# Optimization experiments

Measured on AMD Instinct MI355X. Metric: run time of the kernel, lower is better.

## Reference

```python
import jax, jax.numpy as jnp
import numpy as np

N = 1_000_000
DEG = 10          # max_output_degree
IN = 16           # in_size (must equal rank for the original einsum to be valid)
RANK = 16
OUT = 16


def setup_inputs() -> dict:
    key = jax.random.key(0)
    k_ns, k_u0, k_ur, k_uo = jax.random.split(key, 4)
    neighbour_states = jax.random.normal(k_ns, (N, DEG, IN), dtype=jnp.float32)
    # Original init uses th.rand (uniform [0,1)).
    U0 = jax.random.uniform(k_u0, (IN, RANK), dtype=jnp.float32)
    U_rest = jax.random.uniform(k_ur, (DEG - 1, IN, RANK, RANK), dtype=jnp.float32)
    U_output = jax.random.uniform(k_uo, (RANK, OUT), dtype=jnp.float32)
    return {"neighbour_states": neighbour_states, "U0": U0, "U_rest": U_rest, "U_output": U_output}


def reference(neighbour_states, U0, U_rest, U_output):
    # neighbour_states: [N, DEG, IN]
    h0 = neighbour_states[:, 0, :]                      # [N, IN]
    ris0 = jnp.einsum('bc,nb->nc', U0, h0)              # [N, RANK]
    hs = jnp.moveaxis(neighbour_states[:, 1:, :], 1, 0)  # [DEG-1, N, IN]

    def step(ris, inputs):
        U, h = inputs                                   # U: [IN, RANK, RANK] (IN==RANK), h: [N, IN]
        ris = jnp.einsum('abc,na,nb->nc', U, ris, h)    # [N, RANK]
        return ris, None

    ris, _ = jax.lax.scan(step, ris0, (U_rest, hs))
    h_out = jnp.einsum('ab,na->nb', U_output, ris)      # [N, OUT]
    return h_out
```

## Files before the change

### kernel.cpp

```cpp
#include <hip/hip_runtime.h>

#define NSTEP 9

typedef __attribute__((ext_vector_type(8)))  __bf16 bf16x8;
typedef __attribute__((ext_vector_type(8)))  short  short8;
typedef __attribute__((ext_vector_type(4)))  float  floatx4;

__device__ __forceinline__ unsigned short bf_hi(float x) {
    unsigned u = __float_as_uint(x);
    return (unsigned short)((u + 0x8000u) >> 16);
}
__device__ __forceinline__ float bf_hi_f(float x) {
    unsigned u = __float_as_uint(x);
    return __uint_as_float((u + 0x8000u) & 0xFFFF0000u);
}
__device__ __forceinline__ unsigned short bf_lo(float x) {
    return bf_hi(x - bf_hi_f(x));
}

__device__ __forceinline__ floatx4 mfma16(bf16x8 a, bf16x8 b, floatx4 c) {
    return __builtin_amdgcn_mfma_f32_16x16x32_bf16(a, b, c, 0, 0, 0);
}
__device__ __forceinline__ bf16x8 cvt(short8 s) {
    return __builtin_bit_cast(bf16x8, s);
}

__global__ void prep_kernel(const float* __restrict__ U0,
                            const float* __restrict__ Ur,
                            short8* __restrict__ ws)
{
    const int fb   = blockIdx.x;
    const int lane = threadIdx.x;
    const int q = lane >> 4, c = lane & 15;
    short8 v;
    if (fb == 0) {
#pragma unroll
        for (int j = 0; j < 8; ++j) {
            int k = 8 * q + j;
            int b = (k < 16) ? k : (k - 16);
            float u = U0[b * 16 + c];
            v[j] = (short)((k < 16) ? bf_hi(u) : bf_lo(u));
        }
        ws[lane] = v;
    } else {
        int idx = fb - 1;
        int t   = idx >> 4;
        int r   = idx & 15;
        int ki  = r >> 1, var = r & 1;
        int a   = 4 * q + (ki >> 1);
        int b0  = 8 * (ki & 1);
#pragma unroll
        for (int j = 0; j < 8; ++j) {
            float u = Ur[((t * 16 + a) * 16 + (b0 + j)) * 16 + c];
            v[j] = (short)(var == 0 ? bf_hi(u) : bf_lo(u));
        }
        ws[64 + idx * 64 + lane] = v;
    }
}

__global__ __launch_bounds__(256) void tt_main(
    const float*  __restrict__ ns,
    const short8* __restrict__ Upk,
    const float*  __restrict__ Uo,
    float*        __restrict__ out,
    int n)
{
    const int lane = threadIdx.x & 63;
    const int wv   = threadIdx.x >> 6;
    const int q    = lane >> 4;
    const int nn   = lane & 15;
    const int nb   = blockIdx.x * 128 + wv * 32;
    const int n0   = nb + nn;
    const int n1   = nb + 16 + nn;
    const int c0   = (n0 < n) ? n0 : 0;
    const int c1   = (n1 < n) ? n1 : 0;
    const float* g0 = ns + (size_t)c0 * 160;
    const float* g1 = ns + (size_t)c1 * 160;

    floatx4 acc0, acc1;

    {
        bf16x8 a0 = cvt(Upk[lane]);
        const int o = (q & 1) * 2;
        float4 x0 = ((const float4*)g0)[o], y0 = ((const float4*)g0)[o + 1];
        float4 x1 = ((const float4*)g1)[o], y1 = ((const float4*)g1)[o + 1];
        float h0a[8] = {x0.x,x0.y,x0.z,x0.w,y0.x,y0.y,y0.z,y0.w};
        float h0b[8] = {x1.x,x1.y,x1.z,x1.w,y1.x,y1.y,y1.z,y1.w};
        short8 bh0, bl0, bh1, bl1;
#pragma unroll
        for (int j = 0; j < 8; ++j) {
            bh0[j] = (short)bf_hi(h0a[j]); bl0[j] = (short)bf_lo(h0a[j]);
            bh1[j] = (short)bf_hi(h0b[j]); bl1[j] = (short)bf_lo(h0b[j]);
        }
        floatx4 z = {0.f, 0.f, 0.f, 0.f};
        acc0 = mfma16(a0, cvt(bh0), z);
        acc0 = mfma16(a0, cvt(bl0), acc0);
        acc1 = mfma16(a0, cvt(bh1), z);
        acc1 = mfma16(a0, cvt(bl1), acc1);
    }

#pragma unroll 1
    for (int t = 0; t < NSTEP; ++t) {
        const float4* h40 = (const float4*)(g0 + (t + 1) * 16);
        const float4* h41 = (const float4*)(g1 + (t + 1) * 16);
        float4 A0 = h40[0], A1 = h40[1], A2 = h40[2], A3 = h40[3];
        float4 B0 = h41[0], B1 = h41[1], B2 = h41[2], B3 = h41[3];
        float ha[16] = {A0.x,A0.y,A0.z,A0.w,A1.x,A1.y,A1.z,A1.w,
                        A2.x,A2.y,A2.z,A2.w,A3.x,A3.y,A3.z,A3.w};
        float hb[16] = {B0.x,B0.y,B0.z,B0.w,B1.x,B1.y,B1.z,B1.w,
                        B2.x,B2.y,B2.z,B2.w,B3.x,B3.y,B3.z,B3.w};

        const short8* ub = Upk + 64 + (size_t)t * 1024;
        floatx4 na = {0.f,0.f,0.f,0.f};
        floatx4 nbk = {0.f,0.f,0.f,0.f};
#pragma unroll
        for (int ki = 0; ki < 8; ++ki) {
            bf16x8 uh = cvt(ub[(ki * 2 + 0) * 64 + lane]);
            bf16x8 ul = cvt(ub[(ki * 2 + 1) * 64 + lane]);
            const float r0 = acc0[ki >> 1];
            const float r1 = acc1[ki >> 1];
            const int   b0 = 8 * (ki & 1);
            short8 wh0, wl0, wh1, wl1;
#pragma unroll
            for (int j = 0; j < 8; ++j) {
                float w0 = r0 * ha[b0 + j];
                float w1 = r1 * hb[b0 + j];
                wh0[j] = (short)bf_hi(w0); wl0[j] = (short)bf_lo(w0);
                wh1[j] = (short)bf_hi(w1); wl1[j] = (short)bf_lo(w1);
            }
            na  = mfma16(uh, cvt(wh0), na);
            na  = mfma16(uh, cvt(wl0), na);
            na  = mfma16(ul, cvt(wh0), na);
            nbk = mfma16(uh, cvt(wh1), nbk);
            nbk = mfma16(uh, cvt(wl1), nbk);
            nbk = mfma16(ul, cvt(wh1), nbk);
        }
        acc0 = na;
        acc1 = nbk;
    }

    float po0[16], po1[16];
#pragma unroll
    for (int cc = 0; cc < 16; ++cc) { po0[cc] = 0.f; po1[cc] = 0.f; }
#pragma unroll
    for (int r = 0; r < 4; ++r) {
        const float* urow = Uo + (4 * q + r) * 16;
        float rv0 = acc0[r];
        float rv1 = acc1[r];
#pragma unroll
        for (int cc = 0; cc < 16; ++cc) {
            float u = urow[cc];
            po0[cc] += u * rv0;
            po1[cc] += u * rv1;
        }
    }
#pragma unroll
    for (int cc = 0; cc < 16; ++cc) {
        po0[cc] += __shfl_xor(po0[cc], 16, 64);
        po0[cc] += __shfl_xor(po0[cc], 32, 64);
        po1[cc] += __shfl_xor(po1[cc], 16, 64);
        po1[cc] += __shfl_xor(po1[cc], 32, 64);
    }
    if (n0 < n) {
        float4 sv;
        sv.x = q==0 ? po0[0] : q==1 ? po0[4] : q==2 ? po0[8]  : po0[12];
        sv.y = q==0 ? po0[1] : q==1 ? po0[5] : q==2 ? po0[9]  : po0[13];
        sv.z = q==0 ? po0[2] : q==1 ? po0[6] : q==2 ? po0[10] : po0[14];
        sv.w = q==0 ? po0[3] : q==1 ? po0[7] : q==2 ? po0[11] : po0[15];
        ((float4*)(out + (size_t)n0 * 16))[q] = sv;
    }
    if (n1 < n) {
        float4 sv;
        sv.x = q==0 ? po1[0] : q==1 ? po1[4] : q==2 ? po1[8]  : po1[12];
        sv.y = q==0 ? po1[1] : q==1 ? po1[5] : q==2 ? po1[9]  : po1[13];
        sv.z = q==0 ? po1[2] : q==1 ? po1[6] : q==2 ? po1[10] : po1[14];
        sv.w = q==0 ? po1[3] : q==1 ? po1[7] : q==2 ? po1[11] : po1[15];
        ((float4*)(out + (size_t)n1 * 16))[q] = sv;
    }
}

extern "C" void kernel_launch(void* const* d_in, const int* in_sizes, int n_in,
                              void* d_out, int out_size, void* d_ws, size_t ws_size,
                              hipStream_t stream) {
    const float* ns = (const float*)d_in[0];
    const float* U0 = (const float*)d_in[1];
    const float* Ur = (const float*)d_in[2];
    const float* Uo = (const float*)d_in[3];
    float* out = (float*)d_out;
    const int n = in_sizes[0] / 160;

    short8* wsv = (short8*)d_ws;
    prep_kernel<<<145, 64, 0, stream>>>(U0, Ur, wsv);

    const int blocks = (n + 127) / 128;
    tt_main<<<blocks, 256, 0, stream>>>(ns, wsv, Uo, out, n);
}
```

Before: 1.182 ms.

## Restructure TT recurrence to contract h first with 32x32 MFMA and shuffled ris

The per-step contraction order changes. Before, each lane formed ris*h products, split them into bf16 hi/lo and fed them to 16x16x32 MFMAs. Now h is split into hi/lo once per step and contracted with U using 32x32x16 MFMAs, and the ris weighting is applied afterwards in FP32 with values broadcast by wave shuffles. This removes most of the per-element multiply and bf16-split VALU work and halves the number of h loads per lane. It also prefetches the next step's h slice. The cost is 16 shuffles per step, extra FMA work on the 16-wide MFMA results, and the larger 16-register accumulator.

```diff
diff --git a/kernel.cpp b/kernel.cpp
--- a/kernel.cpp
+++ b/kernel.cpp
@@ -4,7 +4,7 @@
 
 typedef __attribute__((ext_vector_type(8)))  __bf16 bf16x8;
 typedef __attribute__((ext_vector_type(8)))  short  short8;
-typedef __attribute__((ext_vector_type(4)))  float  floatx4;
+typedef __attribute__((ext_vector_type(16))) float  floatx16;
 
 __device__ __forceinline__ unsigned short bf_hi(float x) {
     unsigned u = __float_as_uint(x);
@@ -18,8 +18,8 @@
     return bf_hi(x - bf_hi_f(x));
 }
 
-__device__ __forceinline__ floatx4 mfma16(bf16x8 a, bf16x8 b, floatx4 c) {
-    return __builtin_amdgcn_mfma_f32_16x16x32_bf16(a, b, c, 0, 0, 0);
+__device__ __forceinline__ floatx16 mfma32(bf16x8 a, bf16x8 b, floatx16 c) {
+    return __builtin_amdgcn_mfma_f32_32x32x16_bf16(a, b, c, 0, 0, 0);
 }
 __device__ __forceinline__ bf16x8 cvt(short8 s) {
     return __builtin_bit_cast(bf16x8, s);
@@ -29,33 +29,31 @@
                             const float* __restrict__ Ur,
                             short8* __restrict__ ws)
 {
-    const int fb   = blockIdx.x;
+    const int f    = blockIdx.x;
     const int lane = threadIdx.x;
-    const int q = lane >> 4, c = lane & 15;
+    const int hh = lane >> 5, m = lane & 31;
     short8 v;
-    if (fb == 0) {
+    if (f == 0) {
 #pragma unroll
         for (int j = 0; j < 8; ++j) {
-            int k = 8 * q + j;
-            int b = (k < 16) ? k : (k - 16);
-            float u = U0[b * 16 + c];
-            v[j] = (short)((k < 16) ? bf_hi(u) : bf_lo(u));
+            int b = 8 * hh + j;
+            float u = U0[b * 16 + (m & 15)];
+            v[j] = (short)((m < 16) ? bf_hi(u) : bf_lo(u));
         }
-        ws[lane] = v;
     } else {
-        int idx = fb - 1;
+        int idx = f - 1;
+        int var = idx & 1;
+        int p   = (idx >> 1) & 7;
         int t   = idx >> 4;
-        int r   = idx & 15;
-        int ki  = r >> 1, var = r & 1;
-        int a   = 4 * q + (ki >> 1);
-        int b0  = 8 * (ki & 1);
+        int a   = 2 * p + (m >> 4);
 #pragma unroll
         for (int j = 0; j < 8; ++j) {
-            float u = Ur[((t * 16 + a) * 16 + (b0 + j)) * 16 + c];
-            v[j] = (short)(var == 0 ? bf_hi(u) : bf_lo(u));
+            int b = 8 * hh + j;
+            float u = Ur[((t * 16 + a) * 16 + b) * 16 + (m & 15)];
+            v[j] = (short)(var ? bf_lo(u) : bf_hi(u));
         }
-        ws[64 + idx * 64 + lane] = v;
     }
+    ws[f * 64 + lane] = v;
 }
 
 __global__ __launch_bounds__(256) void tt_main(
@@ -67,115 +65,97 @@
 {
     const int lane = threadIdx.x & 63;
     const int wv   = threadIdx.x >> 6;
-    const int q    = lane >> 4;
-    const int nn   = lane & 15;
+    const int hh   = lane >> 5;
+    const int nn   = lane & 31;
     const int nb   = blockIdx.x * 128 + wv * 32;
     const int n0   = nb + nn;
-    const int n1   = nb + 16 + nn;
-    const int c0   = (n0 < n) ? n0 : 0;
-    const int c1   = (n1 < n) ? n1 : 0;
-    const float* g0 = ns + (size_t)c0 * 160;
-    const float* g1 = ns + (size_t)c1 * 160;
+    const int cn   = (n0 < n) ? n0 : (n - 1);
+    const float* g = ns + (size_t)cn * 160 + hh * 8;
 
-    floatx4 acc0, acc1;
+    floatx16 z;
+#pragma unroll
+    for (int i = 0; i < 16; ++i) z[i] = 0.f;
+
+    float ris[8];
+    float4 px0, px1;
 
     {
         bf16x8 a0 = cvt(Upk[lane]);
-        const int o = (q & 1) * 2;
-        float4 x0 = ((const float4*)g0)[o], y0 = ((const float4*)g0)[o + 1];
-        float4 x1 = ((const float4*)g1)[o], y1 = ((const float4*)g1)[o + 1];
-        float h0a[8] = {x0.x,x0.y,x0.z,x0.w,y0.x,y0.y,y0.z,y0.w};
-        float h0b[8] = {x1.x,x1.y,x1.z,x1.w,y1.x,y1.y,y1.z,y1.w};
-        short8 bh0, bl0, bh1, bl1;
+        float4 x0 = ((const float4*)g)[0];
+        float4 x1 = ((const float4*)g)[1];
+        px0 = ((const float4*)(g + 16))[0];
+        px1 = ((const float4*)(g + 16))[1];
+        float hv[8] = {x0.x,x0.y,x0.z,x0.w,x1.x,x1.y,x1.z,x1.w};
+        short8 bh, bl;
 #pragma unroll
-        for (int j = 0; j < 8; ++j) {
-            bh0[j] = (short)bf_hi(h0a[j]); bl0[j] = (short)bf_lo(h0a[j]);
-            bh1[j] = (short)bf_hi(h0b[j]); bl1[j] = (short)bf_lo(h0b[j]);
-        }
-        floatx4 z = {0.f, 0.f, 0.f, 0.f};
-        acc0 = mfma16(a0, cvt(bh0), z);
-        acc0 = mfma16(a0, cvt(bl0), acc0);
-        acc1 = mfma16(a0, cvt(bh1), z);
-        acc1 = mfma16(a0, cvt(bl1), acc1);
+        for (int j = 0; j < 8; ++j) { bh[j] = (short)bf_hi(hv[j]); bl[j] = (short)bf_lo(hv[j]); }
+        floatx16 D = mfma32(a0, cvt(bh), z);
+        D = mfma32(a0, cvt(bl), D);
+#pragma unroll
+        for (int s = 0; s < 8; ++s) ris[s] = D[s] + D[8 + s];
     }
 
 #pragma unroll 1
     for (int t = 0; t < NSTEP; ++t) {
-        const float4* h40 = (const float4*)(g0 + (t + 1) * 16);
-        const float4* h41 = (const float4*)(g1 + (t + 1) * 16);
-        float4 A0 = h40[0], A1 = h40[1], A2 = h40[2], A3 = h40[3];
-        float4 B0 = h41[0], B1 = h41[1], B2 = h41[2], B3 = h41[3];
-        float ha[16] = {A0.x,A0.y,A0.z,A0.w,A1.x,A1.y,A1.z,A1.w,
-                        A2.x,A2.y,A2.z,A2.w,A3.x,A3.y,A3.z,A3.w};
-        float hb[16] = {B0.x,B0.y,B0.z,B0.w,B1.x,B1.y,B1.z,B1.w,
-                        B2.x,B2.y,B2.z,B2.w,B3.x,B3.y,B3.z,B3.w};
+        float hv[8] = {px0.x,px0.y,px0.z,px0.w,px1.x,px1.y,px1.z,px1.w};
+        if (t + 1 < NSTEP) {
+            px0 = ((const float4*)(g + (t + 2) * 16))[0];
+            px1 = ((const float4*)(g + (t + 2) * 16))[1];
+        }
+        short8 bh, bl;
+#pragma unroll
+        for (int j = 0; j < 8; ++j) { bh[j] = (short)bf_hi(hv[j]); bl[j] = (short)bf_lo(hv[j]); }
+        const bf16x8 vbh = cvt(bh), vbl = cvt(bl);
+
+        float ra[16];
+#pragma unroll
+        for (int a = 0; a < 16; ++a) {
+            const int s   = (a & 3) + 4 * (a >> 3);
+            const int src = ((a >> 2) & 1) * 32 + nn;
+            ra[a] = __shfl(ris[s], src, 64);
+        }
 
         const short8* ub = Upk + 64 + (size_t)t * 1024;
-        floatx4 na = {0.f,0.f,0.f,0.f};
-        floatx4 nbk = {0.f,0.f,0.f,0.f};
+        float rn[8];
 #pragma unroll
-        for (int ki = 0; ki < 8; ++ki) {
-            bf16x8 uh = cvt(ub[(ki * 2 + 0) * 64 + lane]);
-            bf16x8 ul = cvt(ub[(ki * 2 + 1) * 64 + lane]);
-            const float r0 = acc0[ki >> 1];
-            const float r1 = acc1[ki >> 1];
-            const int   b0 = 8 * (ki & 1);
-            short8 wh0, wl0, wh1, wl1;
+        for (int s = 0; s < 8; ++s) rn[s] = 0.f;
 #pragma unroll
-            for (int j = 0; j < 8; ++j) {
-                float w0 = r0 * ha[b0 + j];
-                float w1 = r1 * hb[b0 + j];
-                wh0[j] = (short)bf_hi(w0); wl0[j] = (short)bf_lo(w0);
-                wh1[j] = (short)bf_hi(w1); wl1[j] = (short)bf_lo(w1);
-            }
-            na  = mfma16(uh, cvt(wh0), na);
-            na  = mfma16(uh, cvt(wl0), na);
-            na  = mfma16(ul, cvt(wh0), na);
-            nbk = mfma16(uh, cvt(wh1), nbk);
-            nbk = mfma16(uh, cvt(wl1), nbk);
-            nbk = mfma16(ul, cvt(wh1), nbk);
+        for (int p = 0; p < 8; ++p) {
+            bf16x8 uh = cvt(ub[(2 * p + 0) * 64 + lane]);
+            bf16x8 ul = cvt(ub[(2 * p + 1) * 64 + lane]);
+            floatx16 D = mfma32(uh, vbh, z);
+            D = mfma32(uh, vbl, D);
+            D = mfma32(ul, vbh, D);
+            const float r0 = ra[2 * p];
+            const float r1 = ra[2 * p + 1];
+#pragma unroll
+            for (int s = 0; s < 8; ++s) rn[s] += r0 * D[s] + r1 * D[8 + s];
         }
-        acc0 = na;
-        acc1 = nbk;
+#pragma unroll
+        for (int s = 0; s < 8; ++s) ris[s] = rn[s];
     }
 
-    float po0[16], po1[16];
+    float po[16];
 #pragma unroll
-    for (int cc = 0; cc < 16; ++cc) { po0[cc] = 0.f; po1[cc] = 0.f; }
+    for (int cc = 0; cc < 16; ++cc) po[cc] = 0.f;
 #pragma unroll
-    for (int r = 0; r < 4; ++r) {
-        const float* urow = Uo + (4 * q + r) * 16;
-        float rv0 = acc0[r];
-        float rv1 = acc1[r];
+    for (int s = 0; s < 8; ++s) {
+        const int c = 4 * hh + (s & 3) + 8 * (s >> 2);
+        const float* urow = Uo + c * 16;
+        const float rv = ris[s];
 #pragma unroll
-        for (int cc = 0; cc < 16; ++cc) {
-            float u = urow[cc];
-            po0[cc] += u * rv0;
-            po1[cc] += u * rv1;
-        }
+        for (int cc = 0; cc < 16; ++cc) po[cc] += urow[cc] * rv;
     }
 #pragma unroll
-    for (int cc = 0; cc < 16; ++cc) {
-        po0[cc] += __shfl_xor(po0[cc], 16, 64);
-        po0[cc] += __shfl_xor(po0[cc], 32, 64);
-        po1[cc] += __shfl_xor(po1[cc], 16, 64);
-        po1[cc] += __shfl_xor(po1[cc], 32, 64);
-    }
+    for (int cc = 0; cc < 16; ++cc) po[cc] += __shfl_xor(po[cc], 32, 64);
     if (n0 < n) {
-        float4 sv;
-        sv.x = q==0 ? po0[0] : q==1 ? po0[4] : q==2 ? po0[8]  : po0[12];
-        sv.y = q==0 ? po0[1] : q==1 ? po0[5] : q==2 ? po0[9]  : po0[13];
-        sv.z = q==0 ? po0[2] : q==1 ? po0[6] : q==2 ? po0[10] : po0[14];
-        sv.w = q==0 ? po0[3] : q==1 ? po0[7] : q==2 ? po0[11] : po0[15];
-        ((float4*)(out + (size_t)n0 * 16))[q] = sv;
-    }
-    if (n1 < n) {
-        float4 sv;
-        sv.x = q==0 ? po1[0] : q==1 ? po1[4] : q==2 ? po1[8]  : po1[12];
-        sv.y = q==0 ? po1[1] : q==1 ? po1[5] : q==2 ? po1[9]  : po1[13];
-        sv.z = q==0 ? po1[2] : q==1 ? po1[6] : q==2 ? po1[10] : po1[14];
-        sv.w = q==0 ? po1[3] : q==1 ? po1[7] : q==2 ? po1[11] : po1[15];
-        ((float4*)(out + (size_t)n1 * 16))[q] = sv;
+        const int o = 8 * hh;
+        float4 v0, v1;
+        v0.x = po[o + 0]; v0.y = po[o + 1]; v0.z = po[o + 2]; v0.w = po[o + 3];
+        v1.x = po[o + 4]; v1.y = po[o + 5]; v1.z = po[o + 6]; v1.w = po[o + 7];
+        float4* op = (float4*)(out + (size_t)n0 * 16);
+        op[2 * hh + 0] = v0;
+        op[2 * hh + 1] = v1;
     }
 }
 
```

Result: faster. 1.039 ms (-12.0%).
